# Kernel optimization log

Measured on AMD Instinct MI355X. Metric: run time of the kernel, lower is better.

The kernel has to match this reference:

```python
import jax, jax.numpy as jnp
import numpy as np

GAMMA = 2.0  # init arg gamma
EPS = 1e-8   # torch F.cosine_similarity eps


def setup_inputs() -> dict:
    key = jax.random.key(0)
    k1, k2, k3 = jax.random.split(key, 3)
    B, C, H, W_ = 4, 256, 64, 64
    x = jax.random.normal(k1, (B, C, H, W_), dtype=jnp.float32)
    # 1x1 conv weight [out_c, in_c] and bias
    W = jax.random.normal(k2, (C, C), dtype=jnp.float32) * (1.0 / np.sqrt(C))
    b = jax.random.normal(k3, (C,), dtype=jnp.float32) * 0.01
    return {"x": x, "W": W, "b": b}


def reference(x, W, b):
    B, C, H, W_ = x.shape
    N = H * W_
    xf = x.reshape(B, C, N)                                    # [B,C,N]
    # cosine similarity across channel dim, with torch-style eps clamp
    norm = jnp.maximum(jnp.sqrt(jnp.sum(xf * xf, axis=1)), EPS)  # [B,N]
    xn = xf / norm[:, None, :]                                  # [B,C,N]
    sim = jnp.einsum('bcn,bcm->bnm', xn, xn)                    # [B,N,N]
    sim = jax.nn.relu(sim) ** GAMMA
    # 1x1 conv = per-pixel channel mixing
    t = jnp.einsum('oc,bchw->bohw', W, x) + b[None, :, None, None]
    tf = t.reshape(B, C, N)                                     # [B,C,N]
    # einsum 'b x y h w, b c h w -> b c x y'
    out = jnp.einsum('bnm,bcm->bcn', sim, tf)
    return out.reshape(B, C, H, W_)
```

## Files before the change

### kernel.cpp

```cpp
#include <hip/hip_runtime.h>
#include <stdint.h>

#define CC 256
#define NN 4096

typedef __attribute__((ext_vector_type(8))) short short8;
typedef __attribute__((ext_vector_type(4))) float floatx4;
typedef __attribute__((ext_vector_type(4))) unsigned int uint4v;
typedef __attribute__((ext_vector_type(2))) unsigned int uint2v;

__device__ __forceinline__ unsigned short f2bf(float f) {
    unsigned int u = __builtin_bit_cast(unsigned int, f);
    u = (u + 0x7FFFu + ((u >> 16) & 1u)) >> 16;
    return (unsigned short)u;
}

__device__ __forceinline__ floatx4 mfma16(short8 a, short8 b, floatx4 c) {
    return __builtin_amdgcn_mfma_f32_16x16x32_bf16(a, b, c, 0, 0, 0);
}


__global__ __launch_bounds__(256) void k_trans(const float* __restrict__ x,
                                               unsigned short* __restrict__ xB,
                                               unsigned short* __restrict__ xG,
                                               float* __restrict__ psum) {
    int blk = blockIdx.x;
    int b  = blk >> 8;
    int cc = (blk >> 6) & 3;
    int nc = blk & 63;
    int c0 = cc << 6, n0 = nc << 6;
    __shared__ float tile[64][65];
    __shared__ float red[4][64];
    int t = threadIdx.x;
    {
        int c   = t >> 2;
        int nn4 = (t & 3) << 4;
        const float* src = x + (size_t)(b * CC + c0 + c) * NN + n0 + nn4;
        #pragma unroll
        for (int j = 0; j < 16; j += 4) {
            floatx4 v = *(const floatx4*)(src + j);
            tile[c][nn4 + j + 0] = v[0];
            tile[c][nn4 + j + 1] = v[1];
            tile[c][nn4 + j + 2] = v[2];
            tile[c][nn4 + j + 3] = v[3];
        }
    }
    __syncthreads();
    int g = t >> 6, lane = t & 63, l15 = lane & 15, q = lane >> 4;
    #pragma unroll
    for (int kkl = 0; kkl < 2; ++kkl) {
        unsigned int w[4];
        #pragma unroll
        for (int j = 0; j < 4; ++j) {
            unsigned int lo = f2bf(tile[32 * kkl + 8 * q + 2 * j][16 * g + l15]);
            unsigned int hi = f2bf(tile[32 * kkl + 8 * q + 2 * j + 1][16 * g + l15]);
            w[j] = lo | (hi << 16);
        }
        uint4v p = {w[0], w[1], w[2], w[3]};
        *(uint4v*)(xB + ((size_t)(b * 256 + (n0 >> 4) + g) * 8 + (c0 >> 5) + kkl) * 512
                   + lane * 8) = p;
    }
    #pragma unroll
    for (int kk2 = 0; kk2 < 2; ++kk2) {
        unsigned int w[4];
        #pragma unroll
        for (int j = 0; j < 4; ++j) {
            unsigned int lo = f2bf(tile[16 * g + l15][32 * kk2 + 8 * q + 2 * j]);
            unsigned int hi = f2bf(tile[16 * g + l15][32 * kk2 + 8 * q + 2 * j + 1]);
            w[j] = lo | (hi << 16);
        }
        uint4v p = {w[0], w[1], w[2], w[3]};
        *(uint4v*)(xG + (size_t)(b * 64 + nc) * 16 * 1024
                   + ((size_t)((c0 >> 4) + g)) * 1024 + kk2 * 512 + lane * 8) = p;
    }
    {
        int n  = t & 63;
        int cq = t >> 6;
        float ss = 0.f;
        #pragma unroll
        for (int i = 0; i < 16; ++i) {
            float v = tile[cq * 16 + i][n];
            ss = fmaf(v, v, ss);
        }
        red[cq][n] = ss;
    }
    __syncthreads();
    if (t < 64) {
        float s = red[0][t] + red[1][t] + red[2][t] + red[3][t];
        psum[((size_t)(b * 64 + nc) * 64 + t) * 4 + cc] = s;
    }
}

__global__ __launch_bounds__(256) void k_invwcast(const float* __restrict__ psum,
                                                  float* __restrict__ invn,
                                                  const float* __restrict__ Wm,
                                                  unsigned short* __restrict__ wF) {
    int bid = blockIdx.x;
    int t = threadIdx.x;
    if (bid < 64) {
        int i = bid * 256 + t;
        floatx4 p = *(const floatx4*)(psum + (size_t)i * 4);
        float ss = (p[0] + p[1]) + (p[2] + p[3]);
        invn[i] = 1.f / fmaxf(sqrtf(ss), 1e-8f);
    } else {
        int idx = (bid - 64) * 256 + t;
        int f = idx >> 6, lane = idx & 63;
        int ct = f >> 3, kk = f & 7;
        int l15 = lane & 15, q = lane >> 4;
        const float* src = Wm + (size_t)(16 * ct + l15) * CC + 32 * kk + 8 * q;
        floatx4 a = *(const floatx4*)src;
        floatx4 c = *(const floatx4*)(src + 4);
        unsigned int w0 = f2bf(a[0]) | ((unsigned int)f2bf(a[1]) << 16);
        unsigned int w1 = f2bf(a[2]) | ((unsigned int)f2bf(a[3]) << 16);
        unsigned int w2 = f2bf(c[0]) | ((unsigned int)f2bf(c[1]) << 16);
        unsigned int w3 = f2bf(c[2]) | ((unsigned int)f2bf(c[3]) << 16);
        uint4v p = {w0, w1, w2, w3};
        *(uint4v*)(wF + (size_t)f * 512 + lane * 8) = p;
    }
}

#define FUSED_STEP(IT, BQC, BQN, XGP, XGC, DO_G2)                              \
    {                                                                          \
                \
        _Pragma("unroll")                                                      \
        for (int kk = 0; kk < 8; ++kk)                                         \
            BQN[kk] = *(const short8*)(bqp + kk * 512);                        \
        bqp += 16384;                                                          \
        _Pragma("unroll")                                                      \
        for (int ci = 0; ci < 2; ++ci)                                         \
            _Pragma("unroll")                                                  \
            for (int kk2 = 0; kk2 < 2; ++kk2)                                  \
                XGC[ci][kk2] = *(const short8*)(xgp + ci * 8192 + kk2 * 512);  \
        xgp += 16384;                                                          \
        floatx4 invm4 = *(const floatx4*)invmp;                                \
        invmp += 64;                                                           \
        __builtin_amdgcn_s_setprio(1);                                         \
                  \
        floatx4 s0a = zero4, s0b = zero4, s1a = zero4, s1b = zero4;            \
        _Pragma("unroll")                                                      \
        for (int kk = 0; kk < 8; kk += 2) {                                    \
            s0a = mfma16(BQC[kk],     aq[0][kk],     s0a);                     \
            s1a = mfma16(BQC[kk],     aq[1][kk],     s1a);                     \
            s0b = mfma16(BQC[kk + 1], aq[0][kk + 1], s0b);                     \
            s1b = mfma16(BQC[kk + 1], aq[1][kk + 1], s1b);                     \
        }                                                                      \
                                       \
        if (DO_G2) {                                                           \
            const unsigned short* pbR = pbuf[((IT) - 1) & 1];                  \
            _Pragma("unroll")                                                  \
            for (int kk2 = 0; kk2 < 2; ++kk2)                                  \
                _Pragma("unroll")                                              \
                for (int nqs = 0; nqs < 4; ++nqs) {                            \
                    short8 pbf = *(const short8*)(pbR + (16 * nqs + l15) * 72  \
                                                  + kk2 * 32 + q * 8);         \
                    Zacc[0][nqs] = mfma16(XGP[0][kk2], pbf, Zacc[0][nqs]);     \
                    Zacc[1][nqs] = mfma16(XGP[1][kk2], pbf, Zacc[1][nqs]);     \
                }                                                              \
        }                                                                      \
        __builtin_amdgcn_s_setprio(0);                                         \
                  \
        {                                                                      \
            unsigned short* pbW = pbuf[(IT) & 1];                              \
            _Pragma("unroll")                                                  \
            for (int s = 0; s < 2; ++s) {                                      \
                floatx4 sv = (s == 0) ? (s0a + s0b) : (s1a + s1b);             \
                unsigned int pk0, pk1;                                         \
                float v0 = sv[0] * (invm4[0] * invq[s]);                       \
                float v1 = sv[1] * (invm4[1] * invq[s]);                       \
                float v2 = sv[2] * (invm4[2] * invq[s]);                       \
                float v3 = sv[3] * (invm4[3] * invq[s]);                       \
                v0 = fmaxf(v0, 0.f); v1 = fmaxf(v1, 0.f);                      \
                v2 = fmaxf(v2, 0.f); v3 = fmaxf(v3, 0.f);                      \
                v0 *= v0; v1 *= v1; v2 *= v2; v3 *= v3;                        \
                csum[s] += (v0 + v1) + (v2 + v3);                              \
                pk0 = __byte_perm(__builtin_bit_cast(unsigned int, v0) + 0x8000u, \
                                  __builtin_bit_cast(unsigned int, v1) + 0x8000u, \
                                  0x7632);                                     \
                pk1 = __byte_perm(__builtin_bit_cast(unsigned int, v2) + 0x8000u, \
                                  __builtin_bit_cast(unsigned int, v3) + 0x8000u, \
                                  0x7632);                                     \
                uint2v w2 = {pk0, pk1};                                        \
                *(uint2v*)(pbW + (16 * (2 * np + s) + l15) * 72                \
                           + 16 * ms + 4 * q) = w2;                            \
            }                                                                  \
        }                                                                      \
        asm volatile("s_waitcnt lgkmcnt(0)\n\ts_barrier" ::: "memory");        \
    }

__global__ __launch_bounds__(512, 1) void k_fused(
        const unsigned short* __restrict__ xB,
        const unsigned short* __restrict__ xG,
        const unsigned short* __restrict__ wF,
        const float* __restrict__ bias,
        const float* __restrict__ invn,
        float* __restrict__ out) {
    int blk = blockIdx.x;
    int b  = (blk & 7) >> 1;
    int qt = ((blk >> 3) << 1) | (blk & 1);
    int n0 = qt << 6;
    int t  = threadIdx.x;
    int wv = t >> 6, lane = t & 63;
    int l15 = lane & 15, q = lane >> 4;
    int ms = wv & 3;
    int np = wv >> 2;

    __shared__ unsigned short pbuf[2][64 * 72];
    __shared__ unsigned short zbuf[64 * 264];
    __shared__ float spbuf2[4][64];

    const unsigned short* xBb = xB + (size_t)b * 256 * 8 * 512;
    const unsigned short* xGb = xG + (size_t)b * 64 * 16 * 1024;
    const float* invb = invn + b * NN;

    short8 aq[2][8];
    #pragma unroll
    for (int s = 0; s < 2; ++s)
        #pragma unroll
        for (int kk = 0; kk < 8; ++kk)
            aq[s][kk] = *(const short8*)(xBb
                + ((size_t)((n0 >> 4) + 2 * np + s) * 8 + kk) * 512 + lane * 8);
    float invq[2];
    #pragma unroll
    for (int s = 0; s < 2; ++s) invq[s] = invb[n0 + 16 * (2 * np + s) + l15];

    floatx4 zero4 = {0.f, 0.f, 0.f, 0.f};
    floatx4 Zacc[2][4];
    #pragma unroll
    for (int ci = 0; ci < 2; ++ci)
        #pragma unroll
        for (int nqs = 0; nqs < 4; ++nqs) Zacc[ci][nqs] = zero4;
    float csum[2] = {0.f, 0.f};

    const unsigned short* bqp   = xBb + ms * 4096 + lane * 8;
    const unsigned short* xgp   = xGb + wv * 1024 + lane * 8;
    const float*          invmp = invb + 16 * ms + 4 * q;

    short8 bqA[8], bqB[8];
    short8 xgA[2][2], xgB[2][2];
    #pragma unroll
    for (int kk = 0; kk < 8; ++kk)
        bqA[kk] = *(const short8*)(bqp + kk * 512);
    bqp += 16384;

    FUSED_STEP(0, bqA, bqB, xgB, xgA, false)
    for (int it2 = 0; it2 < 31; ++it2) {
        int itO = 2 * it2 + 1;
        FUSED_STEP(itO, bqB, bqA, xgA, xgB, true)
        int itE = 2 * it2 + 2;
        FUSED_STEP(itE, bqA, bqB, xgB, xgA, true)
    }
    FUSED_STEP(63, bqB, bqA, xgA, xgB, true)
    {
        const unsigned short* pbR = pbuf[1];
        #pragma unroll
        for (int kk2 = 0; kk2 < 2; ++kk2)
            #pragma unroll
            for (int nqs = 0; nqs < 4; ++nqs) {
                short8 pbf = *(const short8*)(pbR + (16 * nqs + l15) * 72
                                              + kk2 * 32 + q * 8);
                Zacc[0][nqs] = mfma16(xgB[0][kk2], pbf, Zacc[0][nqs]);
                Zacc[1][nqs] = mfma16(xgB[1][kk2], pbf, Zacc[1][nqs]);
            }
    }

    #pragma unroll
    for (int s = 0; s < 2; ++s) {
        csum[s] += __shfl_xor(csum[s], 16, 64);
        csum[s] += __shfl_xor(csum[s], 32, 64);
    }

    __syncthreads();
    #pragma unroll
    for (int ci = 0; ci < 2; ++ci) {
        int cct = wv + 8 * ci;
        #pragma unroll
        for (int nqs = 0; nqs < 4; ++nqs)
            #pragma unroll
            for (int i = 0; i < 4; ++i)
                zbuf[(16 * nqs + l15) * 264 + 16 * cct + 4 * q + i] = f2bf(Zacc[ci][nqs][i]);
    }
    if (q == 0) {
        #pragma unroll
        for (int s = 0; s < 2; ++s)
            spbuf2[ms][16 * (2 * np + s) + l15] = csum[s];
    }
    __syncthreads();

    float svals[4];
    #pragma unroll
    for (int nqs = 0; nqs < 4; ++nqs)
        svals[nqs] = spbuf2[0][16 * nqs + l15] + spbuf2[1][16 * nqs + l15]
                   + spbuf2[2][16 * nqs + l15] + spbuf2[3][16 * nqs + l15];

    float* ob = out + (size_t)b * CC * NN;
    floatx4 oa[2][4];
    #pragma unroll
    for (int ci = 0; ci < 2; ++ci) {
        int ct = wv + 8 * ci;
        floatx4 bv = *(const floatx4*)(bias + 16 * ct + 4 * q);
        #pragma unroll
        for (int nqs = 0; nqs < 4; ++nqs)
            #pragma unroll
            for (int i = 0; i < 4; ++i) oa[ci][nqs][i] = bv[i] * svals[nqs];
    }
    #pragma unroll
    for (int kk = 0; kk < 8; ++kk) {
        short8 wf0 = *(const short8*)(wF + (size_t)(wv * 8 + kk) * 512 + lane * 8);
        short8 wf1 = *(const short8*)(wF + (size_t)((wv + 8) * 8 + kk) * 512 + lane * 8);
        #pragma unroll
        for (int nqs = 0; nqs < 4; ++nqs) {
            short8 zf = *(const short8*)(&zbuf[(16 * nqs + l15) * 264 + 32 * kk + 8 * q]);
            oa[0][nqs] = mfma16(wf0, zf, oa[0][nqs]);
            oa[1][nqs] = mfma16(wf1, zf, oa[1][nqs]);
        }
    }
    #pragma unroll
    for (int ci = 0; ci < 2; ++ci) {
        int ct = wv + 8 * ci;
        #pragma unroll
        for (int nqs = 0; nqs < 4; ++nqs)
            #pragma unroll
            for (int i = 0; i < 4; ++i)
                ob[(size_t)(16 * ct + 4 * q + i) * NN + n0 + 16 * nqs + l15] = oa[ci][nqs][i];
    }
}

extern "C" void kernel_launch(void* const* d_in, const int* in_sizes, int n_in,
                              void* d_out, int out_size, void* d_ws, size_t ws_size,
                              hipStream_t stream) {
    const float* x    = (const float*)d_in[0];
    const float* Wm   = (const float*)d_in[1];
    const float* bias = (const float*)d_in[2];
    float* out = (float*)d_out;

    char* ws = (char*)d_ws;
    float* psum         = (float*)ws;
    float* invn         = (float*)(ws + 262144);
    unsigned short* xB  = (unsigned short*)(ws + 262144 + 65536);
    unsigned short* xG  = (unsigned short*)(ws + 262144 + 65536 + 8388608);
    unsigned short* wF  = (unsigned short*)(ws + 262144 + 65536 + 2 * 8388608);

    k_trans   <<<1024, 256, 0, stream>>>(x, xB, xG, psum);
    k_invwcast<<<96,   256, 0, stream>>>(psum, invn, Wm, wF);
    k_fused   <<<256,  512, 0, stream>>>(xB, xG, wF, bias, invn, out);
}
```

Baseline: 164.3 us.

## Fold weight cast into transpose kernel and compute inverse norms in fused kernel

Removes the separate inverse-norm and weight-cast launch. The weight bf16 cast moves into extra blocks of the transpose kernel, and each fused-kernel block now rebuilds the per-batch inverse norms from psum into a 16KB shared array. This saves one launch and its dependency gap. It also swaps the bf16 packing for a cheaper round-half-up byte-permute, and moves the S-tile MFMAs after the Z-accumulation MFMAs with setprio removed. The costs are redundant inverse-norm work in every block, extra shared memory that may reduce occupancy, and slightly different rounding on ties.

```diff
diff --git a/kernel.cpp b/kernel.cpp
--- a/kernel.cpp
+++ b/kernel.cpp
@@ -15,6 +15,11 @@
     return (unsigned short)u;
 }
 
+__device__ __forceinline__ unsigned int pack2bf(float lo, float hi) {
+    return __byte_perm(__builtin_bit_cast(unsigned int, lo) + 0x8000u,
+                       __builtin_bit_cast(unsigned int, hi) + 0x8000u, 0x7632);
+}
+
 __device__ __forceinline__ floatx4 mfma16(short8 a, short8 b, floatx4 c) {
     return __builtin_amdgcn_mfma_f32_16x16x32_bf16(a, b, c, 0, 0, 0);
 }
@@ -23,15 +28,30 @@
 __global__ __launch_bounds__(256) void k_trans(const float* __restrict__ x,
                                                unsigned short* __restrict__ xB,
                                                unsigned short* __restrict__ xG,
-                                               float* __restrict__ psum) {
+                                               float* __restrict__ psum,
+                                               const float* __restrict__ Wm,
+                                               unsigned short* __restrict__ wF) {
     int blk = blockIdx.x;
+    int t = threadIdx.x;
+    if (blk >= 1024) {
+        int idx = (blk - 1024) * 256 + t;
+        int f = idx >> 6, lane = idx & 63;
+        int ct = f >> 3, kk = f & 7;
+        int l15 = lane & 15, q = lane >> 4;
+        const float* src = Wm + (size_t)(16 * ct + l15) * CC + 32 * kk + 8 * q;
+        floatx4 a = *(const floatx4*)src;
+        floatx4 c = *(const floatx4*)(src + 4);
+        uint4v p = {pack2bf(a[0], a[1]), pack2bf(a[2], a[3]),
+                    pack2bf(c[0], c[1]), pack2bf(c[2], c[3])};
+        *(uint4v*)(wF + (size_t)f * 512 + lane * 8) = p;
+        return;
+    }
     int b  = blk >> 8;
     int cc = (blk >> 6) & 3;
     int nc = blk & 63;
     int c0 = cc << 6, n0 = nc << 6;
     __shared__ float tile[64][65];
     __shared__ float red[4][64];
-    int t = threadIdx.x;
     {
         int c   = t >> 2;
         int nn4 = (t & 3) << 4;
@@ -51,11 +71,9 @@
     for (int kkl = 0; kkl < 2; ++kkl) {
         unsigned int w[4];
         #pragma unroll
-        for (int j = 0; j < 4; ++j) {
-            unsigned int lo = f2bf(tile[32 * kkl + 8 * q + 2 * j][16 * g + l15]);
-            unsigned int hi = f2bf(tile[32 * kkl + 8 * q + 2 * j + 1][16 * g + l15]);
-            w[j] = lo | (hi << 16);
-        }
+        for (int j = 0; j < 4; ++j)
+            w[j] = pack2bf(tile[32 * kkl + 8 * q + 2 * j][16 * g + l15],
+                           tile[32 * kkl + 8 * q + 2 * j + 1][16 * g + l15]);
         uint4v p = {w[0], w[1], w[2], w[3]};
         *(uint4v*)(xB + ((size_t)(b * 256 + (n0 >> 4) + g) * 8 + (c0 >> 5) + kkl) * 512
                    + lane * 8) = p;
@@ -64,11 +82,9 @@
     for (int kk2 = 0; kk2 < 2; ++kk2) {
         unsigned int w[4];
         #pragma unroll
-        for (int j = 0; j < 4; ++j) {
-            unsigned int lo = f2bf(tile[16 * g + l15][32 * kk2 + 8 * q + 2 * j]);
-            unsigned int hi = f2bf(tile[16 * g + l15][32 * kk2 + 8 * q + 2 * j + 1]);
-            w[j] = lo | (hi << 16);
-        }
+        for (int j = 0; j < 4; ++j)
+            w[j] = pack2bf(tile[16 * g + l15][32 * kk2 + 8 * q + 2 * j],
+                           tile[16 * g + l15][32 * kk2 + 8 * q + 2 * j + 1]);
         uint4v p = {w[0], w[1], w[2], w[3]};
         *(uint4v*)(xG + (size_t)(b * 64 + nc) * 16 * 1024
                    + ((size_t)((c0 >> 4) + g)) * 1024 + kk2 * 512 + lane * 8) = p;
@@ -88,34 +104,6 @@
     if (t < 64) {
         float s = red[0][t] + red[1][t] + red[2][t] + red[3][t];
         psum[((size_t)(b * 64 + nc) * 64 + t) * 4 + cc] = s;
-    }
-}
-
-__global__ __launch_bounds__(256) void k_invwcast(const float* __restrict__ psum,
-                                                  float* __restrict__ invn,
-                                                  const float* __restrict__ Wm,
-                                                  unsigned short* __restrict__ wF) {
-    int bid = blockIdx.x;
-    int t = threadIdx.x;
-    if (bid < 64) {
-        int i = bid * 256 + t;
-        floatx4 p = *(const floatx4*)(psum + (size_t)i * 4);
-        float ss = (p[0] + p[1]) + (p[2] + p[3]);
-        invn[i] = 1.f / fmaxf(sqrtf(ss), 1e-8f);
-    } else {
-        int idx = (bid - 64) * 256 + t;
-        int f = idx >> 6, lane = idx & 63;
-        int ct = f >> 3, kk = f & 7;
-        int l15 = lane & 15, q = lane >> 4;
-        const float* src = Wm + (size_t)(16 * ct + l15) * CC + 32 * kk + 8 * q;
-        floatx4 a = *(const floatx4*)src;
-        floatx4 c = *(const floatx4*)(src + 4);
-        unsigned int w0 = f2bf(a[0]) | ((unsigned int)f2bf(a[1]) << 16);
-        unsigned int w1 = f2bf(a[2]) | ((unsigned int)f2bf(a[3]) << 16);
-        unsigned int w2 = f2bf(c[0]) | ((unsigned int)f2bf(c[1]) << 16);
-        unsigned int w3 = f2bf(c[2]) | ((unsigned int)f2bf(c[3]) << 16);
-        uint4v p = {w0, w1, w2, w3};
-        *(uint4v*)(wF + (size_t)f * 512 + lane * 8) = p;
     }
 }
 
@@ -134,16 +122,6 @@
         xgp += 16384;                                                          \
         floatx4 invm4 = *(const floatx4*)invmp;                                \
         invmp += 64;                                                           \
-        __builtin_amdgcn_s_setprio(1);                                         \
-                  \
-        floatx4 s0a = zero4, s0b = zero4, s1a = zero4, s1b = zero4;            \
-        _Pragma("unroll")                                                      \
-        for (int kk = 0; kk < 8; kk += 2) {                                    \
-            s0a = mfma16(BQC[kk],     aq[0][kk],     s0a);                     \
-            s1a = mfma16(BQC[kk],     aq[1][kk],     s1a);                     \
-            s0b = mfma16(BQC[kk + 1], aq[0][kk + 1], s0b);                     \
-            s1b = mfma16(BQC[kk + 1], aq[1][kk + 1], s1b);                     \
-        }                                                                      \
                                        \
         if (DO_G2) {                                                           \
             const unsigned short* pbR = pbuf[((IT) - 1) & 1];                  \
@@ -157,7 +135,15 @@
                     Zacc[1][nqs] = mfma16(XGP[1][kk2], pbf, Zacc[1][nqs]);     \
                 }                                                              \
         }                                                                      \
-        __builtin_amdgcn_s_setprio(0);                                         \
+                  \
+        floatx4 s0a = zero4, s0b = zero4, s1a = zero4, s1b = zero4;            \
+        _Pragma("unroll")                                                      \
+        for (int kk = 0; kk < 8; kk += 2) {                                    \
+            s0a = mfma16(BQC[kk],     aq[0][kk],     s0a);                     \
+            s1a = mfma16(BQC[kk],     aq[1][kk],     s1a);                     \
+            s0b = mfma16(BQC[kk + 1], aq[0][kk + 1], s0b);                     \
+            s1b = mfma16(BQC[kk + 1], aq[1][kk + 1], s1b);                     \
+        }                                                                      \
                   \
         {                                                                      \
             unsigned short* pbW = pbuf[(IT) & 1];                              \
@@ -192,7 +178,7 @@
         const unsigned short* __restrict__ xG,
         const unsigned short* __restrict__ wF,
         const float* __restrict__ bias,
-        const float* __restrict__ invn,
+        const float* __restrict__ psum,
         float* __restrict__ out) {
     int blk = blockIdx.x;
     int b  = (blk & 7) >> 1;
@@ -207,10 +193,21 @@
     __shared__ unsigned short pbuf[2][64 * 72];
     __shared__ unsigned short zbuf[64 * 264];
     __shared__ float spbuf2[4][64];
+    __shared__ float invl[4096];
 
     const unsigned short* xBb = xB + (size_t)b * 256 * 8 * 512;
     const unsigned short* xGb = xG + (size_t)b * 64 * 16 * 1024;
-    const float* invb = invn + b * NN;
+
+    {
+        const float* pb = psum + (size_t)b * NN * 4;
+        #pragma unroll
+        for (int i = 0; i < 8; ++i) {
+            int p = t + i * 512;
+            floatx4 ps = *(const floatx4*)(pb + (size_t)p * 4);
+            float ss = (ps[0] + ps[1]) + (ps[2] + ps[3]);
+            invl[p] = 1.f / fmaxf(sqrtf(ss), 1e-8f);
+        }
+    }
 
     short8 aq[2][8];
     #pragma unroll
@@ -219,9 +216,6 @@
         for (int kk = 0; kk < 8; ++kk)
             aq[s][kk] = *(const short8*)(xBb
                 + ((size_t)((n0 >> 4) + 2 * np + s) * 8 + kk) * 512 + lane * 8);
-    float invq[2];
-    #pragma unroll
-    for (int s = 0; s < 2; ++s) invq[s] = invb[n0 + 16 * (2 * np + s) + l15];
 
     floatx4 zero4 = {0.f, 0.f, 0.f, 0.f};
     floatx4 Zacc[2][4];
@@ -233,7 +227,6 @@
 
     const unsigned short* bqp   = xBb + ms * 4096 + lane * 8;
     const unsigned short* xgp   = xGb + wv * 1024 + lane * 8;
-    const float*          invmp = invb + 16 * ms + 4 * q;
 
     short8 bqA[8], bqB[8];
     short8 xgA[2][2], xgB[2][2];
@@ -241,6 +234,12 @@
     for (int kk = 0; kk < 8; ++kk)
         bqA[kk] = *(const short8*)(bqp + kk * 512);
     bqp += 16384;
+
+    __syncthreads();
+    float invq[2];
+    #pragma unroll
+    for (int s = 0; s < 2; ++s) invq[s] = invl[n0 + 16 * (2 * np + s) + l15];
+    const float* invmp = invl + 16 * ms + 4 * q;
 
     FUSED_STEP(0, bqA, bqB, xgB, xgA, false)
     for (int it2 = 0; it2 < 31; ++it2) {
@@ -335,12 +334,10 @@
 
     char* ws = (char*)d_ws;
     float* psum         = (float*)ws;
-    float* invn         = (float*)(ws + 262144);
     unsigned short* xB  = (unsigned short*)(ws + 262144 + 65536);
     unsigned short* xG  = (unsigned short*)(ws + 262144 + 65536 + 8388608);
     unsigned short* wF  = (unsigned short*)(ws + 262144 + 65536 + 2 * 8388608);
 
-    k_trans   <<<1024, 256, 0, stream>>>(x, xB, xG, psum);
-    k_invwcast<<<96,   256, 0, stream>>>(psum, invn, Wm, wF);
-    k_fused   <<<256,  512, 0, stream>>>(xB, xG, wF, bias, invn, out);
-}
+    k_trans <<<1056, 256, 0, stream>>>(x, xB, xG, psum, Wm, wF);
+    k_fused <<<256,  512, 0, stream>>>(xB, xG, wF, bias, psum, out);
+}
```

After: 157.8 us. 4.0% less time.
